# Performance work log

Hardware: AMD Instinct MI355X
Metric: run time of the kernel (lower is better)

## Reference

```python
import jax, jax.numpy as jnp
import numpy as np

B, L, CIN, COUT, HEADS = 8, 2048, 256, 256, 4
HD = COUT // HEADS
NEG_SLOPE = 0.2


def setup_inputs() -> dict:
    key = jax.random.key(0)
    k1, k2, k3, k4, k5 = jax.random.split(key, 5)
    x = jax.random.normal(k1, (B, L, CIN), dtype=jnp.float32)
    adj_mask = jax.random.randint(k2, (B, L, L), 0, 2) > 0  # bool [B,L,L]
    W = jax.random.normal(k3, (COUT, CIN), dtype=jnp.float32) * (1.0 / np.sqrt(CIN))
    att_src = jax.random.normal(k4, (1, HEADS, 1, HD), dtype=jnp.float32) * 0.1
    att_dst = jax.random.normal(k5, (1, HEADS, 1, HD), dtype=jnp.float32) * 0.1
    return {"x": x, "adj_mask": adj_mask, "W": W, "att_src": att_src, "att_dst": att_dst}


def reference(x, adj_mask, W, att_src, att_dst):
    Bb, Ll, _ = x.shape
    # linear projection (no bias), split heads: [B, H, L, D]
    h = jnp.einsum('blc,oc->blo', x, W).reshape(Bb, Ll, HEADS, HD).transpose(0, 2, 1, 3)
    # additive GAT scores
    a_src = jnp.sum(h * att_src, axis=-1, keepdims=True)          # [B,H,L,1]
    a_dst = jnp.sum(h * att_dst, axis=-1, keepdims=True)          # [B,H,L,1]
    e = a_src + jnp.swapaxes(a_dst, 2, 3)                          # [B,H,L,L]
    e = jnp.where(e >= 0, e, NEG_SLOPE * e)                        # leaky relu
    fill = jnp.finfo(e.dtype).min
    e = jnp.where(adj_mask[:, None, :, :], e, fill)                # mask non-edges
    alpha = jax.nn.softmax(e, axis=-1)                             # [B,H,L,L]
    # dropout is identity in eval/reference mode
    out = jnp.einsum('bhij,bhjd->bhid', alpha, h)                  # [B,H,L,D]
    return out.transpose(0, 2, 1, 3).reshape(Bb, Ll, COUT)
```

## Files before the change

### kernel.cpp

```cpp
#include <hip/hip_runtime.h>

#define B_ 8
#define L_ 2048
#define CIN_ 256
#define COUT_ 256
#define HEADS_ 4
#define HD_ 64
#define NEG_SLOPE_ 0.2f
#define LOG2E_ 1.4426950408889634f

#define TI 32
#define TJ 64
#define NJT (L_ / TJ)

typedef __attribute__((ext_vector_type(4))) float f32x4;
typedef __attribute__((ext_vector_type(8))) __bf16 bf16x8;
typedef __attribute__((ext_vector_type(4))) __bf16 bf16x4;


__global__ __launch_bounds__(256, 4)
void pack_kernel(const int* __restrict__ adj, unsigned long long* __restrict__ abits) {
  const size_t wid = ((size_t)blockIdx.x * 256 + threadIdx.x) >> 6;
  const int lane = threadIdx.x & 63;
  const int* p = adj + wid * 256 + lane;
  unsigned long long b0 = __ballot(p[0]   != 0);
  unsigned long long b1 = __ballot(p[64]  != 0);
  unsigned long long b2 = __ballot(p[128] != 0);
  unsigned long long b3 = __ballot(p[192] != 0);
  if (lane == 0) {
    ulonglong2 v01; v01.x = b0; v01.y = b1;
    ulonglong2 v23; v23.x = b2; v23.y = b3;
    *(ulonglong2*)(abits + wid * 4)     = v01;
    *(ulonglong2*)(abits + wid * 4 + 2) = v23;
  }
}

__global__ __launch_bounds__(256, 2)
void proj_kernel(const float* __restrict__ x, const float* __restrict__ W,
                 const float* __restrict__ att_src, const float* __restrict__ att_dst,
                 __bf16* __restrict__ hF, float* __restrict__ a_src,
                 float* __restrict__ a_dst) {
  __shared__ __align__(16) __bf16 Wl[COUT_][80];
  __shared__ __align__(16) __bf16 Al[2][2][512];

  const int tid = threadIdx.x;
  const int r0 = blockIdx.x * TI;
  const int b  = r0 >> 11;
  const int l0 = r0 & (L_ - 1);

  const int w = tid >> 6, lane = tid & 63, col = lane & 15, q = lane >> 4;
  const int si = tid >> 3, soct = tid & 7;
  const int wn = tid >> 2, wkq = tid & 3;

  f32x4 acc[2][4];
#pragma unroll
  for (int mt = 0; mt < 2; ++mt)
#pragma unroll
    for (int nt = 0; nt < 4; ++nt) acc[mt][nt] = (f32x4)0.f;

  for (int kc = 0; kc < CIN_ / 64; ++kc) {
    __syncthreads();
#pragma unroll
    for (int rg = 0; rg < 4; ++rg) {
      const int row = rg * 64 + wn;
      const float4* ws = (const float4*)(W + (size_t)row * CIN_ + kc * 64 + wkq * 16);
#pragma unroll
      for (int u = 0; u < 4; ++u) {
        float4 f = ws[u];
        bf16x4 v;
        v[0] = (__bf16)f.x; v[1] = (__bf16)f.y; v[2] = (__bf16)f.z; v[3] = (__bf16)f.w;
        *(bf16x4*)&Wl[row][wkq * 16 + u * 4] = v;
      }
    }
    {
      const float4* xs = (const float4*)(x + (size_t)(r0 + si) * CIN_ + kc * 64 + soct * 8);
      float4 f0 = xs[0], f1 = xs[1];
      bf16x8 v;
      v[0] = (__bf16)f0.x; v[1] = (__bf16)f0.y; v[2] = (__bf16)f0.z; v[3] = (__bf16)f0.w;
      v[4] = (__bf16)f1.x; v[5] = (__bf16)f1.y; v[6] = (__bf16)f1.z; v[7] = (__bf16)f1.w;
      *(bf16x8*)&Al[si >> 4][soct >> 2][(((soct & 3) << 4) + (si & 15)) << 3] = v;
    }
    __syncthreads();

    bf16x8 af[2][2], bfr[2][4];
#pragma unroll
    for (int mt = 0; mt < 2; ++mt)
#pragma unroll
      for (int kt = 0; kt < 2; ++kt)
        af[mt][kt] = *(const bf16x8*)&Al[mt][kt][lane << 3];
#pragma unroll
    for (int kt = 0; kt < 2; ++kt)
#pragma unroll
      for (int nt = 0; nt < 4; ++nt)
        bfr[kt][nt] = *(const bf16x8*)&Wl[w * 64 + nt * 16 + col][kt * 32 + q * 8];
#pragma unroll
    for (int kt = 0; kt < 2; ++kt)
#pragma unroll
      for (int mt = 0; mt < 2; ++mt)
#pragma unroll
        for (int nt = 0; nt < 4; ++nt)
          acc[mt][nt] = __builtin_amdgcn_mfma_f32_16x16x32_bf16(
              af[mt][kt], bfr[kt][nt], acc[mt][nt], 0, 0, 0);
  }

  float asv[4], adv[4];
#pragma unroll
  for (int nt = 0; nt < 4; ++nt) {
    asv[nt] = att_src[w * 64 + nt * 16 + col];
    adv[nt] = att_dst[w * 64 + nt * 16 + col];
  }
#pragma unroll
  for (int mt = 0; mt < 2; ++mt)
#pragma unroll
    for (int reg = 0; reg < 4; ++reg) {
      float s = 0.f, d = 0.f;
#pragma unroll
      for (int nt = 0; nt < 4; ++nt) {
        s = fmaf(acc[mt][nt][reg], asv[nt], s);
        d = fmaf(acc[mt][nt][reg], adv[nt], d);
      }
      s += __shfl_xor(s, 1, 64); d += __shfl_xor(d, 1, 64);
      s += __shfl_xor(s, 2, 64); d += __shfl_xor(d, 2, 64);
      s += __shfl_xor(s, 4, 64); d += __shfl_xor(d, 4, 64);
      s += __shfl_xor(s, 8, 64); d += __shfl_xor(d, 8, 64);
      if (col == 0) {
        int il = mt * 16 + q * 4 + reg;
        a_src[((size_t)(b * HEADS_ + w) << 11) + l0 + il] = s * LOG2E_;
        a_dst[((size_t)(b * HEADS_ + w) << 11) + l0 + il] = d * LOG2E_;
      }
    }

  {
    const int jt_p = l0 >> 6;
    const int kt_p = (l0 >> 5) & 1;
    const int qhi = q >> 1, qlo = q & 1;
#pragma unroll
    for (int mt = 0; mt < 2; ++mt) {
      const int qp = mt * 2 + qhi;
#pragma unroll
      for (int nt = 0; nt < 4; ++nt) {
        bf16x4 v;
        v[0] = (__bf16)acc[mt][nt][0];
        v[1] = (__bf16)acc[mt][nt][1];
        v[2] = (__bf16)acc[mt][nt][2];
        v[3] = (__bf16)acc[mt][nt][3];
        const size_t off =
            ((((size_t)(b * HEADS_ + w) * 32 + jt_p) * 2 + kt_p) * 4 + nt) * 512 +
            (qp * 16 + col) * 8 + qlo * 4;
        *(bf16x4*)(hF + off) = v;
      }
    }
  }
}

__global__ __launch_bounds__(256, 4)
void attn_kernel(const __bf16* __restrict__ hF, const float* __restrict__ a_src,
                 const float* __restrict__ a_dst,
                 const unsigned long long* __restrict__ abits,
                 float* __restrict__ out) {
  const int tid = threadIdx.x;
  const int b  = blockIdx.x & 7;
  const int i0 = (blockIdx.x >> 3) * 32;

  const int w = tid >> 6, lane = tid & 63, col = lane & 15, q = lane >> 4;

  const size_t hl = (size_t)(b * HEADS_ + w);
  const float asr[2] = {a_src[(hl << 11) + i0 + col],
                        a_src[(hl << 11) + i0 + 16 + col]};
  const float* adb = a_dst + (hl << 11) + q * 8;
  const __bf16* hb = hF + hl * 131072 + lane * 8;
  const unsigned long long* bp0 = abits + (((size_t)b << 11) + i0 + col) * 32;
  const unsigned long long* bp1 = bp0 + (16 * 32);

  f32x4 acc[2][4];
#pragma unroll
  for (int mt = 0; mt < 2; ++mt)
#pragma unroll
    for (int nt = 0; nt < 4; ++nt) acc[mt][nt] = (f32x4)0.f;
  float lacc[2] = {0.f, 0.f};

  for (int jt = 0; jt < NJT; ++jt) {
    bf16x8 cb[2][4];
#pragma unroll
    for (int kt = 0; kt < 2; ++kt)
#pragma unroll
      for (int nt = 0; nt < 4; ++nt)
        cb[kt][nt] = *(const bf16x8*)(hb + jt * 4096 + (kt * 4 + nt) * 512);
    float4 cd[2][2];
#pragma unroll
    for (int kt = 0; kt < 2; ++kt) {
      cd[kt][0] = *(const float4*)(adb + jt * 64 + kt * 32);
      cd[kt][1] = *(const float4*)(adb + jt * 64 + kt * 32 + 4);
    }
    const unsigned long long cw[2] = {bp0[jt], bp1[jt]};

#pragma unroll
    for (int mt = 0; mt < 2; ++mt) {
      bf16x8 av[2];
#pragma unroll
      for (int kt = 0; kt < 2; ++kt) {
        const unsigned int tsh = ((unsigned int)(cw[mt] >> (kt * 32))) >> (q * 8);
        const float dd[8] = {cd[kt][0].x, cd[kt][0].y, cd[kt][0].z, cd[kt][0].w,
                             cd[kt][1].x, cd[kt][1].y, cd[kt][1].z, cd[kt][1].w};
        float ls = 0.f;
#pragma unroll
        for (int e = 0; e < 8; ++e) {
          float t = asr[mt] + dd[e];
          t = fmaxf(t, NEG_SLOPE_ * t);
          float p = ((tsh >> e) & 1u) ? __builtin_exp2f(t) : 0.f;
          ls += p;
          av[kt][e] = (__bf16)p;
        }
        lacc[mt] += ls;
      }
#pragma unroll
      for (int kt = 0; kt < 2; ++kt)
#pragma unroll
        for (int nt = 0; nt < 4; ++nt)
          acc[mt][nt] = __builtin_amdgcn_mfma_f32_16x16x32_bf16(
              av[kt], cb[kt][nt], acc[mt][nt], 0, 0, 0);
    }
  }

#pragma unroll
  for (int mt = 0; mt < 2; ++mt) {
    lacc[mt] += __shfl_xor(lacc[mt], 16, 64);
    lacc[mt] += __shfl_xor(lacc[mt], 32, 64);
  }

#pragma unroll
  for (int mt = 0; mt < 2; ++mt)
#pragma unroll
    for (int reg = 0; reg < 4; ++reg) {
      const int m = q * 4 + reg;
      const float linv = 1.0f / __shfl(lacc[mt], m, 64);
      const size_t orow =
          ((size_t)(b * L_ + i0 + mt * 16 + m)) * COUT_ + w * 64;
#pragma unroll
      for (int nt = 0; nt < 4; ++nt)
        out[orow + nt * 16 + col] = acc[mt][nt][reg] * linv;
    }
}

extern "C" void kernel_launch(void* const* d_in, const int* in_sizes, int n_in,
                              void* d_out, int out_size, void* d_ws, size_t ws_size,
                              hipStream_t stream) {
  const float* x       = (const float*)d_in[0];
  const int*   adj     = (const int*)d_in[1];
  const float* W       = (const float*)d_in[2];
  const float* att_src = (const float*)d_in[3];
  const float* att_dst = (const float*)d_in[4];
  float* out = (float*)d_out;

  char* ws = (char*)d_ws;
  __bf16* hF = (__bf16*)ws;
  float* a_src = (float*)(ws + (8u << 20));
  float* a_dst = (float*)(ws + (8u << 20) + (256u << 10));
  unsigned long long* abits =
      (unsigned long long*)(ws + (8u << 20) + (512u << 10));

  pack_kernel<<<(B_ * L_ * (L_ / 256)) / 4, 256, 0, stream>>>(adj, abits);
  proj_kernel<<<(B_ * L_) / TI, 256, 0, stream>>>(x, W, att_src, att_dst, hF, a_src, a_dst);
  attn_kernel<<<B_ * (L_ / 32), 256, 0, stream>>>(hF, a_src, a_dst, abits, out);
}
```

Before: 283.1 us.

## Transpose adjacency bitmask, prefetch next tile, compute row sums via MFMA

The pack kernel now writes the adjacency bitmask transposed, so that for each 64-column block consecutive rows are contiguous and the attention kernel's per-lane mask loads coalesce. The attention kernel prefetches the next tile's mask words and a_dst values into registers, and reorders its MFMAs. It replaces the scalar exp-sum plus shuffle reduction with an extra MFMA against a ones vector, which also puts each row sum directly in the output register layout. Launch bounds occupancy drops from 4 to 2 to make room for the extra registers. The row sum now uses bf16-rounded probabilities, and the transposed pack stores are scattered.

New measurement: 290.7 us. 1.03x slower.

```diff
diff --git a/kernel.cpp b/kernel.cpp
--- a/kernel.cpp
+++ b/kernel.cpp
@@ -19,7 +19,7 @@
 
 
 __global__ __launch_bounds__(256, 4)
-void pack_kernel(const int* __restrict__ adj, unsigned long long* __restrict__ abits) {
+void pack_kernel(const int* __restrict__ adj, unsigned long long* __restrict__ abitsT) {
   const size_t wid = ((size_t)blockIdx.x * 256 + threadIdx.x) >> 6;
   const int lane = threadIdx.x & 63;
   const int* p = adj + wid * 256 + lane;
@@ -28,10 +28,14 @@
   unsigned long long b2 = __ballot(p[128] != 0);
   unsigned long long b3 = __ballot(p[192] != 0);
   if (lane == 0) {
-    ulonglong2 v01; v01.x = b0; v01.y = b1;
-    ulonglong2 v23; v23.x = b2; v23.y = b3;
-    *(ulonglong2*)(abits + wid * 4)     = v01;
-    *(ulonglong2*)(abits + wid * 4 + 2) = v23;
+    const size_t row = wid >> 3;
+    const int jw0 = (int)(wid & 7) * 4;
+    const size_t bb = row >> 11, l = row & 2047;
+    unsigned long long* dst = abitsT + (bb << 16) + l;
+    dst[(size_t)(jw0 + 0) << 11] = b0;
+    dst[(size_t)(jw0 + 1) << 11] = b1;
+    dst[(size_t)(jw0 + 2) << 11] = b2;
+    dst[(size_t)(jw0 + 3) << 11] = b3;
   }
 }
 
@@ -153,10 +157,10 @@
   }
 }
 
-__global__ __launch_bounds__(256, 4)
+__global__ __launch_bounds__(256, 2)
 void attn_kernel(const __bf16* __restrict__ hF, const float* __restrict__ a_src,
                  const float* __restrict__ a_dst,
-                 const unsigned long long* __restrict__ abits,
+                 const unsigned long long* __restrict__ abitsT,
                  float* __restrict__ out) {
   const int tid = threadIdx.x;
   const int b  = blockIdx.x & 7;
@@ -169,15 +173,27 @@
                         a_src[(hl << 11) + i0 + 16 + col]};
   const float* adb = a_dst + (hl << 11) + q * 8;
   const __bf16* hb = hF + hl * 131072 + lane * 8;
-  const unsigned long long* bp0 = abits + (((size_t)b << 11) + i0 + col) * 32;
-  const unsigned long long* bp1 = bp0 + (16 * 32);
-
-  f32x4 acc[2][4];
-#pragma unroll
-  for (int mt = 0; mt < 2; ++mt)
+  const unsigned long long* mb = abitsT + ((size_t)b << 16) + i0 + col;
+
+  bf16x8 bones;
+#pragma unroll
+  for (int e = 0; e < 8; ++e) bones[e] = (__bf16)1.0f;
+
+  f32x4 acc[2][4], accl[2];
+#pragma unroll
+  for (int mt = 0; mt < 2; ++mt) {
+    accl[mt] = (f32x4)0.f;
 #pragma unroll
     for (int nt = 0; nt < 4; ++nt) acc[mt][nt] = (f32x4)0.f;
-  float lacc[2] = {0.f, 0.f};
+  }
+
+  unsigned long long cm0 = mb[0], cm1 = mb[16];
+  float4 cd[2][2];
+#pragma unroll
+  for (int kt = 0; kt < 2; ++kt) {
+    cd[kt][0] = *(const float4*)(adb + kt * 32);
+    cd[kt][1] = *(const float4*)(adb + kt * 32 + 4);
+  }
 
   for (int jt = 0; jt < NJT; ++jt) {
     bf16x8 cb[2][4];
@@ -186,46 +202,54 @@
 #pragma unroll
       for (int nt = 0; nt < 4; ++nt)
         cb[kt][nt] = *(const bf16x8*)(hb + jt * 4096 + (kt * 4 + nt) * 512);
-    float4 cd[2][2];
+
+    const int jn = (jt < NJT - 1) ? jt + 1 : jt;
+    const unsigned long long nm0 = mb[(size_t)jn << 11];
+    const unsigned long long nm1 = mb[((size_t)jn << 11) + 16];
+    float4 nd[2][2];
 #pragma unroll
     for (int kt = 0; kt < 2; ++kt) {
-      cd[kt][0] = *(const float4*)(adb + jt * 64 + kt * 32);
-      cd[kt][1] = *(const float4*)(adb + jt * 64 + kt * 32 + 4);
-    }
-    const unsigned long long cw[2] = {bp0[jt], bp1[jt]};
-
+      nd[kt][0] = *(const float4*)(adb + jn * 64 + kt * 32);
+      nd[kt][1] = *(const float4*)(adb + jn * 64 + kt * 32 + 4);
+    }
+
+    bf16x8 av[2][2];
 #pragma unroll
     for (int mt = 0; mt < 2; ++mt) {
-      bf16x8 av[2];
+      const unsigned long long bw = mt ? cm1 : cm0;
 #pragma unroll
       for (int kt = 0; kt < 2; ++kt) {
-        const unsigned int tsh = ((unsigned int)(cw[mt] >> (kt * 32))) >> (q * 8);
+        const unsigned int tsh = ((unsigned int)(bw >> (kt * 32))) >> (q * 8);
         const float dd[8] = {cd[kt][0].x, cd[kt][0].y, cd[kt][0].z, cd[kt][0].w,
                              cd[kt][1].x, cd[kt][1].y, cd[kt][1].z, cd[kt][1].w};
-        float ls = 0.f;
 #pragma unroll
         for (int e = 0; e < 8; ++e) {
           float t = asr[mt] + dd[e];
           t = fmaxf(t, NEG_SLOPE_ * t);
           float p = ((tsh >> e) & 1u) ? __builtin_exp2f(t) : 0.f;
-          ls += p;
-          av[kt][e] = (__bf16)p;
+          av[mt][kt][e] = (__bf16)p;
         }
-        lacc[mt] += ls;
-      }
-#pragma unroll
-      for (int kt = 0; kt < 2; ++kt)
+      }
+    }
+
+#pragma unroll
+    for (int kt = 0; kt < 2; ++kt)
+#pragma unroll
+      for (int mt = 0; mt < 2; ++mt) {
 #pragma unroll
         for (int nt = 0; nt < 4; ++nt)
           acc[mt][nt] = __builtin_amdgcn_mfma_f32_16x16x32_bf16(
-              av[kt], cb[kt][nt], acc[mt][nt], 0, 0, 0);
-    }
-  }
-
-#pragma unroll
-  for (int mt = 0; mt < 2; ++mt) {
-    lacc[mt] += __shfl_xor(lacc[mt], 16, 64);
-    lacc[mt] += __shfl_xor(lacc[mt], 32, 64);
+              av[mt][kt], cb[kt][nt], acc[mt][nt], 0, 0, 0);
+        accl[mt] = __builtin_amdgcn_mfma_f32_16x16x32_bf16(
+            av[mt][kt], bones, accl[mt], 0, 0, 0);
+      }
+
+    cm0 = nm0; cm1 = nm1;
+#pragma unroll
+    for (int kt = 0; kt < 2; ++kt) {
+      cd[kt][0] = nd[kt][0];
+      cd[kt][1] = nd[kt][1];
+    }
   }
 
 #pragma unroll
@@ -233,7 +257,7 @@
 #pragma unroll
     for (int reg = 0; reg < 4; ++reg) {
       const int m = q * 4 + reg;
-      const float linv = 1.0f / __shfl(lacc[mt], m, 64);
+      const float linv = 1.0f / accl[mt][reg];
       const size_t orow =
           ((size_t)(b * L_ + i0 + mt * 16 + m)) * COUT_ + w * 64;
 #pragma unroll
@@ -256,10 +280,10 @@
   __bf16* hF = (__bf16*)ws;
   float* a_src = (float*)(ws + (8u << 20));
   float* a_dst = (float*)(ws + (8u << 20) + (256u << 10));
-  unsigned long long* abits =
+  unsigned long long* abitsT =
       (unsigned long long*)(ws + (8u << 20) + (512u << 10));
 
-  pack_kernel<<<(B_ * L_ * (L_ / 256)) / 4, 256, 0, stream>>>(adj, abits);
+  pack_kernel<<<(B_ * L_ * (L_ / 256)) / 4, 256, 0, stream>>>(adj, abitsT);
   proj_kernel<<<(B_ * L_) / TI, 256, 0, stream>>>(x, W, att_src, att_dst, hF, a_src, a_dst);
-  attn_kernel<<<B_ * (L_ / 32), 256, 0, stream>>>(hF, a_src, a_dst, abits, out);
-}
+  attn_kernel<<<B_ * (L_ / 32), 256, 0, stream>>>(hF, a_src, a_dst, abitsT, out);
+}
```
